# Optimization experiments

Measured on AMD Instinct MI355X. Metric: run time of the kernel, lower is better.

## Reference

```python
import jax, jax.numpy as jnp
import numpy as np

MAX_ITER = 10
TAU = 1.0


def setup_inputs() -> dict:
    key = jax.random.key(0)
    k1, k2, k3 = jax.random.split(key, 3)
    B, R, C = 64, 1024, 1024
    s = jax.random.normal(k1, (B, R, C), dtype=jnp.float32)
    # nrows <= ncols per batch => no transposed_batch branch in the original
    nrows = jax.random.randint(k2, (B,), 128, 512).astype(jnp.int32)
    ncols = jax.random.randint(k3, (B,), 512, C + 1).astype(jnp.int32)
    return {"s": s, "nrows": nrows, "ncols": ncols}


def _masked_lse(x, mask, axis):
    """logsumexp over `axis` restricted to mask==True; finite-safe everywhere.
    Equivalent to torch.logsumexp after writing -inf into masked-out entries,
    but keeps all values finite so grads are clean."""
    neg = jnp.asarray(-1e30, x.dtype)
    m = jax.lax.stop_gradient(jnp.max(jnp.where(mask, x, neg), axis=axis, keepdims=True))
    e = jnp.where(mask, jnp.exp(jnp.where(mask, x, m) - m), jnp.zeros((), x.dtype))
    sum_e = jnp.sum(e, axis=axis, keepdims=True)
    any_m = jnp.any(mask, axis=axis, keepdims=True)
    return m + jnp.log(jnp.where(any_m, sum_e, jnp.ones((), x.dtype)))


def _sinkhorn(s, nrows, ncols):
    B, R, C = s.shape
    row_mask = (jnp.arange(R)[None, :] < nrows[:, None])[:, :, None]  # [B,R,1]
    col_mask = (jnp.arange(C)[None, :] < ncols[:, None])[:, None, :]  # [B,1,C]
    valid = row_mask & col_mask                                        # [B,R,C]
    log_s = s / TAU
    # Alternating row/col normalization in log space. In the original, entries
    # outside [nrows,ncols] are set to -inf and ignored by logsumexp; here we
    # keep them finite and mask inside the logsumexp, which is the same math
    # on the valid region, and we zero the invalid region at the end (exp(-inf)=0).
    for i in range(MAX_ITER):
        if i % 2 == 0:  # row normalization
            lse = _masked_lse(log_s, valid, axis=2)          # [B,R,1]
            log_s = log_s - jnp.where(row_mask, lse, 0.0)
        else:           # col normalization
            lse = _masked_lse(log_s, valid, axis=1)          # [B,1,C]
            log_s = log_s - jnp.where(col_mask, lse, 0.0)
    return jnp.where(valid, jnp.exp(log_s), jnp.zeros((), s.dtype))


def reference(s, nrows, ncols):
    return _sinkhorn(s, nrows, ncols)
```

## Files before the change

kernel.cpp:

```cpp
#include <hip/hip_runtime.h>
#include <hip/hip_fp16.h>


#define B_DIM 64
#define RCH 32
#define NCH 16

__device__ __forceinline__ float fast_rcp(float x) {
#if __has_builtin(__builtin_amdgcn_rcpf)
    return __builtin_amdgcn_rcpf(x);
#else
    return 1.0f / x;
#endif
}

__device__ __forceinline__ float wave_sum(float x) {
    #pragma unroll
    for (int off = 1; off < 64; off <<= 1) x += __shfl_xor(x, off);
    return x;
}

__device__ __forceinline__ void phase2_col(
    const __half* __restrict__ E, const float* __restrict__ a_lds,
    float* __restrict__ cls,
    int b, int r0, int nr, int nc, int t, float* __restrict__ cs_cur)
{
    const int c0 = (t & 127) << 3;
    const int rsub = t >> 7;
    float acc0 = 0.f, acc1 = 0.f, acc2 = 0.f, acc3 = 0.f;
    float acc4 = 0.f, acc5 = 0.f, acc6 = 0.f, acc7 = 0.f;
    if (c0 < nc) {
        const int rs = r0 + (rsub << 3);
        const __half* __restrict__ Eb = E + ((size_t)b << 19) + c0;
        #pragma unroll
        for (int k = 0; k < 8; ++k) {
            const int r = rs + k;
            const float4 p = *reinterpret_cast<const float4*>(Eb + ((size_t)r << 10));
            const __half2* h = reinterpret_cast<const __half2*>(&p);
            const float av = a_lds[r - r0];
            const float2 f0 = __half22float2(h[0]);
            const float2 f1 = __half22float2(h[1]);
            const float2 f2 = __half22float2(h[2]);
            const float2 f3 = __half22float2(h[3]);
            acc0 = fmaf(f0.x, av, acc0); acc1 = fmaf(f0.y, av, acc1);
            acc2 = fmaf(f1.x, av, acc2); acc3 = fmaf(f1.y, av, acc3);
            acc4 = fmaf(f2.x, av, acc4); acc5 = fmaf(f2.y, av, acc5);
            acc6 = fmaf(f3.x, av, acc6); acc7 = fmaf(f3.y, av, acc7);
        }
    }
    float* dst = cls + (rsub << 10) + c0;
    *reinterpret_cast<float4*>(dst)     = make_float4(acc0, acc1, acc2, acc3);
    *reinterpret_cast<float4*>(dst + 4) = make_float4(acc4, acc5, acc6, acc7);
    __syncthreads();
    #pragma unroll
    for (int k = 0; k < 2; ++k) {
        const int c = t + (k << 9);
        const float v = cls[c] + cls[1024 + c] + cls[2048 + c] + cls[3072 + c];
        if (v != 0.f) atomicAdd(cs_cur + (b << 10) + c, v);
    }
}

__global__ __launch_bounds__(512) void pair_first(
    const float* __restrict__ s, const int* __restrict__ nrows,
    const int* __restrict__ ncols, __half* __restrict__ E,
    float* __restrict__ a, float* __restrict__ cs_cur,
    float* __restrict__ cs_next)
{
    const int b = blockIdx.y;
    const int rc = blockIdx.x;
    const int t = threadIdx.x;
    if (t < 64) cs_next[(b << 10) + (rc << 6) + t] = 0.f;

    const int nr = nrows[b];
    const int r0 = rc << 5;
    if (r0 >= nr) return;
    const int nc = ncols[b];

    __shared__ float a_lds[RCH];
    __shared__ float cls[4 * 1024];

    const int wave = t >> 6;
    const int lane = t & 63;
    const int cbase = lane << 4;
    const bool cOK = cbase < nc;

    #pragma unroll 1
    for (int k = 0; k < 4; ++k) {
        const int r = r0 + (wave << 2) + k;
        float sum = 0.f;
        if (r < nr && cOK) {
            const float* __restrict__ srow =
                s + ((size_t)b << 20) + ((size_t)r << 10) + cbase;
            __half* __restrict__ erow =
                E + ((size_t)b << 19) + ((size_t)r << 10) + cbase;
            float e[16];
            #pragma unroll
            for (int q = 0; q < 4; ++q) {
                const float4 x = *reinterpret_cast<const float4*>(srow + (q << 2));
                e[4 * q + 0] = __expf(x.x); e[4 * q + 1] = __expf(x.y);
                e[4 * q + 2] = __expf(x.z); e[4 * q + 3] = __expf(x.w);
            }
            #pragma unroll
            for (int j = 0; j < 16; ++j)
                if (cbase + j >= nc) e[j] = 0.f;
            __half2 h[8];
            #pragma unroll
            for (int q = 0; q < 8; ++q)
                h[q] = __floats2half2_rn(e[2 * q], e[2 * q + 1]);
            *reinterpret_cast<float4*>(erow)     = *reinterpret_cast<const float4*>(&h[0]);
            *reinterpret_cast<float4*>(erow + 8) = *reinterpret_cast<const float4*>(&h[4]);
            #pragma unroll
            for (int j = 0; j < 16; ++j) sum += e[j];
        }
        sum = wave_sum(sum);
        if (lane == 0) a_lds[(wave << 2) + k] = (r < nr) ? 1.0f / sum : 0.f;
    }
    __syncthreads();
    if (t < RCH) a[(b << 9) + r0 + t] = a_lds[t];

    phase2_col(E, a_lds, cls, b, r0, nr, nc, t, cs_cur);
}

__global__ __launch_bounds__(512) void pair_mid(
    const __half* __restrict__ E, const int* __restrict__ nrows,
    const int* __restrict__ ncols, const float* __restrict__ cs_prev,
    float* __restrict__ a, float* __restrict__ cs_cur,
    float* __restrict__ cs_next)
{
    const int b = blockIdx.y;
    const int rc = blockIdx.x;
    const int t = threadIdx.x;
    if (t < 64) cs_next[(b << 10) + (rc << 6) + t] = 0.f;

    const int nr = nrows[b];
    const int r0 = rc << 5;
    if (r0 >= nr) return;
    const int nc = ncols[b];

    __shared__ float a_lds[RCH];
    __shared__ float cls[4 * 1024];

    const int wave = t >> 6;
    const int lane = t & 63;
    const int cbase = lane << 4;
    const bool cOK = cbase < nc;

    float w[16];
    if (cOK) {
        const float* __restrict__ csp = cs_prev + (b << 10) + cbase;
        #pragma unroll
        for (int q = 0; q < 4; ++q) {
            const float4 c4 = *reinterpret_cast<const float4*>(csp + (q << 2));
            w[4 * q + 0] = (cbase + 4 * q + 0 < nc) ? fast_rcp(c4.x) : 0.f;
            w[4 * q + 1] = (cbase + 4 * q + 1 < nc) ? fast_rcp(c4.y) : 0.f;
            w[4 * q + 2] = (cbase + 4 * q + 2 < nc) ? fast_rcp(c4.z) : 0.f;
            w[4 * q + 3] = (cbase + 4 * q + 3 < nc) ? fast_rcp(c4.w) : 0.f;
        }
    }

    #pragma unroll 1
    for (int k = 0; k < 4; ++k) {
        const int r = r0 + (wave << 2) + k;
        float s0 = 0.f, s1 = 0.f;
        if (r < nr && cOK) {
            const __half* __restrict__ erow =
                E + ((size_t)b << 19) + ((size_t)r << 10) + cbase;
            float4 p0 = *reinterpret_cast<const float4*>(erow);
            float4 p1 = *reinterpret_cast<const float4*>(erow + 8);
            const __half2* h0 = reinterpret_cast<const __half2*>(&p0);
            const __half2* h1 = reinterpret_cast<const __half2*>(&p1);
            #pragma unroll
            for (int q = 0; q < 4; ++q) {
                const float2 f = __half22float2(h0[q]);
                s0 = fmaf(f.x, w[2 * q], s0);
                s1 = fmaf(f.y, w[2 * q + 1], s1);
            }
            #pragma unroll
            for (int q = 0; q < 4; ++q) {
                const float2 f = __half22float2(h1[q]);
                s0 = fmaf(f.x, w[8 + 2 * q], s0);
                s1 = fmaf(f.y, w[8 + 2 * q + 1], s1);
            }
        }
        const float sum = wave_sum(s0 + s1);
        if (lane == 0) a_lds[(wave << 2) + k] = (r < nr) ? 1.0f / sum : 0.f;
    }
    __syncthreads();
    if (t < RCH) a[(b << 9) + r0 + t] = a_lds[t];

    phase2_col(E, a_lds, cls, b, r0, nr, nc, t, cs_cur);
}

__global__ __launch_bounds__(256) void out_step_f(
    const __half* __restrict__ E, const int* __restrict__ nrows,
    const int* __restrict__ ncols, const float* __restrict__ a,
    const float* __restrict__ cs, float* __restrict__ out)
{
    const int g = (blockIdx.x << 8) + threadIdx.x;
    const int b = g >> 18;
    const int rem = g & 262143;
    const int r = rem >> 8;
    const int c0 = (rem & 255) << 2;
    const int nr = nrows[b];
    const int nc = ncols[b];
    float4 o = make_float4(0.f, 0.f, 0.f, 0.f);
    if (r < nr && c0 < nc) {
        const float ar = a[(b << 9) + r];
        float2 pk = *reinterpret_cast<const float2*>(
            E + ((size_t)b << 19) + ((size_t)r << 10) + c0);
        const float2 f01 = __half22float2(reinterpret_cast<const __half2*>(&pk)[0]);
        const float2 f23 = __half22float2(reinterpret_cast<const __half2*>(&pk)[1]);
        const float4 c4 = *reinterpret_cast<const float4*>(cs + (b << 10) + c0);
        o.x = f01.x * ar * fast_rcp(c4.x);
        o.y = (c0 + 1 < nc) ? f01.y * ar * fast_rcp(c4.y) : 0.f;
        o.z = (c0 + 2 < nc) ? f23.x * ar * fast_rcp(c4.z) : 0.f;
        o.w = (c0 + 3 < nc) ? f23.y * ar * fast_rcp(c4.w) : 0.f;
    }
    reinterpret_cast<float4*>(out)[g] = o;
}


__global__ __launch_bounds__(256) void row_step_lg(
    const float* __restrict__ s, const int* __restrict__ nrows,
    const int* __restrict__ ncols, const float* __restrict__ vlog,
    const int use_v, float* __restrict__ u)
{
    const int b = blockIdx.y, r = blockIdx.x;
    const int nr = nrows[b];
    if (r >= nr) return;
    const int nc = ncols[b];
    const int t = threadIdx.x, c0 = t << 2;
    float sum = 0.f;
    if (c0 < nc) {
        const float4 x = reinterpret_cast<const float4*>(
            s + ((size_t)b << 20) + ((size_t)r << 10))[t];
        float4 vv = make_float4(0.f, 0.f, 0.f, 0.f);
        if (use_v) vv = reinterpret_cast<const float4*>(vlog + ((size_t)b << 10))[t];
        sum  = (c0 + 0 < nc) ? __expf(x.x - vv.x) : 0.f;
        sum += (c0 + 1 < nc) ? __expf(x.y - vv.y) : 0.f;
        sum += (c0 + 2 < nc) ? __expf(x.z - vv.z) : 0.f;
        sum += (c0 + 3 < nc) ? __expf(x.w - vv.w) : 0.f;
    }
    #pragma unroll
    for (int off = 1; off < 64; off <<= 1) sum += __shfl_xor(sum, off);
    __shared__ float ss[4];
    if ((t & 63) == 0) ss[t >> 6] = sum;
    __syncthreads();
    if (t == 0) u[((size_t)b << 9) + r] = __logf(ss[0] + ss[1] + ss[2] + ss[3]);
}

__global__ __launch_bounds__(256) void col_step_lg(
    const float* __restrict__ s, const int* __restrict__ nrows,
    const int* __restrict__ ncols, const float* __restrict__ u,
    float* __restrict__ partial)
{
    const int b = blockIdx.z, rc = blockIdx.y;
    const int nr = nrows[b];
    const int r0 = rc << 6;
    if (r0 >= nr) return;
    const int nc = ncols[b];
    const int c = (blockIdx.x << 8) + threadIdx.x;
    float sum = 0.f;
    if (c < nc) {
        const int rend = min(r0 + 64, nr);
        const float* __restrict__ sb = s + ((size_t)b << 20) + c;
        const float* __restrict__ ub = u + ((size_t)b << 9);
        float s0 = 0.f, s1 = 0.f, s2 = 0.f, s3 = 0.f;
        int r = r0;
        for (; r + 4 <= rend; r += 4) {
            s0 += __expf(sb[(size_t)(r + 0) << 10] - ub[r + 0]);
            s1 += __expf(sb[(size_t)(r + 1) << 10] - ub[r + 1]);
            s2 += __expf(sb[(size_t)(r + 2) << 10] - ub[r + 2]);
            s3 += __expf(sb[(size_t)(r + 3) << 10] - ub[r + 3]);
        }
        for (; r < rend; ++r) s0 += __expf(sb[(size_t)r << 10] - ub[r]);
        sum = (s0 + s1) + (s2 + s3);
    }
    partial[(((size_t)b << 3) + rc) << 10 | c] = sum;
}

__global__ __launch_bounds__(256) void col_fin_lg(
    const int* __restrict__ nrows, const float* __restrict__ partial,
    float* __restrict__ vlog)
{
    const int idx = (blockIdx.x << 8) + threadIdx.x;
    const int b = idx >> 10;
    const int nch = (nrows[b] + 63) >> 6;
    const float* __restrict__ p = partial + ((size_t)(b << 3) << 10) + (idx & 1023);
    float sum = 0.f;
    for (int k = 0; k < nch; ++k) sum += p[(size_t)k << 10];
    vlog[idx] = (sum > 0.f) ? __logf(sum) : 0.f;
}

__global__ __launch_bounds__(256) void out_step_lg(
    const float* __restrict__ s, const int* __restrict__ nrows,
    const int* __restrict__ ncols, const float* __restrict__ u,
    const float* __restrict__ vlog, float* __restrict__ out)
{
    const size_t total4 = (size_t)B_DIM * 1024 * 1024 / 4;
    float4* out4 = reinterpret_cast<float4*>(out);
    const float4* s4 = reinterpret_cast<const float4*>(s);
    for (size_t i = (size_t)blockIdx.x * blockDim.x + threadIdx.x; i < total4;
         i += (size_t)gridDim.x * blockDim.x) {
        const int b = (int)(i >> 18);
        const int rem = (int)(i & 262143);
        const int r = rem >> 8;
        const int c0 = (rem & 255) << 2;
        const int nr = nrows[b], nc = ncols[b];
        float4 o;
        if (r >= nr || c0 >= nc) {
            o = make_float4(0.f, 0.f, 0.f, 0.f);
        } else {
            float4 x = s4[i];
            const float ur = u[((size_t)b << 9) + r];
            const float* vb = vlog + ((size_t)b << 10);
            o.x = (c0 + 0 < nc) ? __expf(x.x - ur - vb[c0 + 0]) : 0.f;
            o.y = (c0 + 1 < nc) ? __expf(x.y - ur - vb[c0 + 1]) : 0.f;
            o.z = (c0 + 2 < nc) ? __expf(x.z - ur - vb[c0 + 2]) : 0.f;
            o.w = (c0 + 3 < nc) ? __expf(x.w - ur - vb[c0 + 3]) : 0.f;
        }
        out4[i] = o;
    }
}


extern "C" void kernel_launch(void* const* d_in, const int* in_sizes, int n_in,
                              void* d_out, int out_size, void* d_ws, size_t ws_size,
                              hipStream_t stream) {
    const float* s = (const float*)d_in[0];
    const int* nrows = (const int*)d_in[1];
    const int* ncols = (const int*)d_in[2];
    float* out = (float*)d_out;

    const size_t E_BYTES = (size_t)B_DIM * 512 * 1024 * 2;
    const size_t CS_ELEMS = (size_t)B_DIM * 1024;
    const size_t NEED = E_BYTES + (size_t)B_DIM * 512 * 4 + 3 * CS_ELEMS * 4;

    if (ws_size >= NEED) {
        __half* E = (__half*)d_ws;
        float* a = (float*)((char*)d_ws + E_BYTES);
        float* cs0 = a + B_DIM * 512;
        float* cs1 = cs0 + CS_ELEMS;
        float* cs2 = cs1 + CS_ELEMS;

        hipMemsetAsync(cs0, 0, CS_ELEMS * sizeof(float), stream);

        const dim3 grid(NCH, B_DIM);
        pair_first<<<grid, 512, 0, stream>>>(s, nrows, ncols, E, a, cs0, cs1);
        pair_mid<<<grid, 512, 0, stream>>>(E, nrows, ncols, cs0, a, cs1, cs2);
        pair_mid<<<grid, 512, 0, stream>>>(E, nrows, ncols, cs1, a, cs2, cs0);
        pair_mid<<<grid, 512, 0, stream>>>(E, nrows, ncols, cs2, a, cs0, cs1);
        pair_mid<<<grid, 512, 0, stream>>>(E, nrows, ncols, cs0, a, cs1, cs2);
        out_step_f<<<65536, 256, 0, stream>>>(E, nrows, ncols, a, cs1, out);
    } else {
        float* u = (float*)d_ws;
        float* vlog = u + (size_t)B_DIM * 512;
        float* partial = vlog + (size_t)B_DIM * 1024;
        const dim3 rowGrid(512, B_DIM);
        const dim3 colGrid(4, 8, B_DIM);
        for (int it = 0; it < 5; ++it) {
            row_step_lg<<<rowGrid, 256, 0, stream>>>(s, nrows, ncols, vlog, it, u);
            col_step_lg<<<colGrid, 256, 0, stream>>>(s, nrows, ncols, u, partial);
            col_fin_lg<<<256, 256, 0, stream>>>(nrows, partial, vlog);
        }
        out_step_lg<<<4096, 256, 0, stream>>>(s, nrows, ncols, u, vlog, out);
    }
}
```

Baseline: 161.4 us.

## Stage E tile in LDS for column pass and swizzle blocks across XCDs

The row pass now writes its 32x1024 fp16 tile of E into shared memory, and the column-sum phase reads from LDS instead of reloading E from global memory. This removes the second global or L2 read of each tile per iteration. Block indices are also remapped so each XCD handles a contiguous group of batches, for L2 locality in both the pair kernels and the output kernel. The LDS footprint grows to 64KB per block, which may limit occupancy. Each thread now issues two atomics instead of the previous LDS pre-reduction.

```diff
diff --git a/kernel.cpp b/kernel.cpp
--- a/kernel.cpp
+++ b/kernel.cpp
@@ -4,7 +4,6 @@
 
 #define B_DIM 64
 #define RCH 32
-#define NCH 16
 
 __device__ __forceinline__ float fast_rcp(float x) {
 #if __has_builtin(__builtin_amdgcn_rcpf)
@@ -21,43 +20,30 @@
 }
 
 __device__ __forceinline__ void phase2_col(
-    const __half* __restrict__ E, const float* __restrict__ a_lds,
-    float* __restrict__ cls,
-    int b, int r0, int nr, int nc, int t, float* __restrict__ cs_cur)
-{
-    const int c0 = (t & 127) << 3;
-    const int rsub = t >> 7;
-    float acc0 = 0.f, acc1 = 0.f, acc2 = 0.f, acc3 = 0.f;
-    float acc4 = 0.f, acc5 = 0.f, acc6 = 0.f, acc7 = 0.f;
-    if (c0 < nc) {
-        const int rs = r0 + (rsub << 3);
-        const __half* __restrict__ Eb = E + ((size_t)b << 19) + c0;
-        #pragma unroll
-        for (int k = 0; k < 8; ++k) {
-            const int r = rs + k;
-            const float4 p = *reinterpret_cast<const float4*>(Eb + ((size_t)r << 10));
-            const __half2* h = reinterpret_cast<const __half2*>(&p);
-            const float av = a_lds[r - r0];
-            const float2 f0 = __half22float2(h[0]);
-            const float2 f1 = __half22float2(h[1]);
-            const float2 f2 = __half22float2(h[2]);
-            const float2 f3 = __half22float2(h[3]);
-            acc0 = fmaf(f0.x, av, acc0); acc1 = fmaf(f0.y, av, acc1);
-            acc2 = fmaf(f1.x, av, acc2); acc3 = fmaf(f1.y, av, acc3);
-            acc4 = fmaf(f2.x, av, acc4); acc5 = fmaf(f2.y, av, acc5);
-            acc6 = fmaf(f3.x, av, acc6); acc7 = fmaf(f3.y, av, acc7);
-        }
-    }
-    float* dst = cls + (rsub << 10) + c0;
-    *reinterpret_cast<float4*>(dst)     = make_float4(acc0, acc1, acc2, acc3);
-    *reinterpret_cast<float4*>(dst + 4) = make_float4(acc4, acc5, acc6, acc7);
-    __syncthreads();
+    const __half* __restrict__ e_lds,
+    const float* __restrict__ a_lds, int b, int nc, int t,
+    float* __restrict__ cs_cur)
+{
+    const int c0 = t << 1;
+    if (c0 >= nc) return;
+    float s0 = 0.f, s1 = 0.f;
     #pragma unroll
-    for (int k = 0; k < 2; ++k) {
-        const int c = t + (k << 9);
-        const float v = cls[c] + cls[1024 + c] + cls[2048 + c] + cls[3072 + c];
-        if (v != 0.f) atomicAdd(cs_cur + (b << 10) + c, v);
-    }
+    for (int rr = 0; rr < RCH; ++rr) {
+        const float2 f = __half22float2(
+            *reinterpret_cast<const __half2*>(e_lds + (rr << 10) + c0));
+        const float av = a_lds[rr];
+        s0 = fmaf(f.x, av, s0);
+        s1 = fmaf(f.y, av, s1);
+    }
+    if (s0 != 0.f) atomicAdd(cs_cur + (b << 10) + c0, s0);
+    if (s1 != 0.f) atomicAdd(cs_cur + (b << 10) + c0 + 1, s1);
+}
+
+__device__ __forceinline__ void decode_pair_bid(int bid, int& b, int& rc) {
+    const int xcd = bid & 7;
+    const int j = bid >> 3;
+    rc = j & 15;
+    b = (xcd << 3) | (j >> 4);
 }
 
 __global__ __launch_bounds__(512) void pair_first(
@@ -66,8 +52,8 @@
     float* __restrict__ a, float* __restrict__ cs_cur,
     float* __restrict__ cs_next)
 {
-    const int b = blockIdx.y;
-    const int rc = blockIdx.x;
+    int b, rc;
+    decode_pair_bid(blockIdx.x, b, rc);
     const int t = threadIdx.x;
     if (t < 64) cs_next[(b << 10) + (rc << 6) + t] = 0.f;
 
@@ -76,8 +62,8 @@
     if (r0 >= nr) return;
     const int nc = ncols[b];
 
+    __shared__ __half e_lds[RCH * 1024];
     __shared__ float a_lds[RCH];
-    __shared__ float cls[4 * 1024];
 
     const int wave = t >> 6;
     const int lane = t & 63;
@@ -86,13 +72,13 @@
 
     #pragma unroll 1
     for (int k = 0; k < 4; ++k) {
-        const int r = r0 + (wave << 2) + k;
+        const int rr = (wave << 2) + k;
+        const int r = r0 + rr;
         float sum = 0.f;
+        __half2 h[8];
         if (r < nr && cOK) {
             const float* __restrict__ srow =
                 s + ((size_t)b << 20) + ((size_t)r << 10) + cbase;
-            __half* __restrict__ erow =
-                E + ((size_t)b << 19) + ((size_t)r << 10) + cbase;
             float e[16];
             #pragma unroll
             for (int q = 0; q < 4; ++q) {
@@ -103,22 +89,29 @@
             #pragma unroll
             for (int j = 0; j < 16; ++j)
                 if (cbase + j >= nc) e[j] = 0.f;
-            __half2 h[8];
             #pragma unroll
             for (int q = 0; q < 8; ++q)
                 h[q] = __floats2half2_rn(e[2 * q], e[2 * q + 1]);
+            __half* __restrict__ erow =
+                E + ((size_t)b << 19) + ((size_t)r << 10) + cbase;
             *reinterpret_cast<float4*>(erow)     = *reinterpret_cast<const float4*>(&h[0]);
             *reinterpret_cast<float4*>(erow + 8) = *reinterpret_cast<const float4*>(&h[4]);
             #pragma unroll
             for (int j = 0; j < 16; ++j) sum += e[j];
-        }
+        } else {
+            #pragma unroll
+            for (int q = 0; q < 8; ++q) h[q] = __floats2half2_rn(0.f, 0.f);
+        }
+        __half* dst = e_lds + (rr << 10) + cbase;
+        *reinterpret_cast<float4*>(dst)     = *reinterpret_cast<const float4*>(&h[0]);
+        *reinterpret_cast<float4*>(dst + 8) = *reinterpret_cast<const float4*>(&h[4]);
         sum = wave_sum(sum);
-        if (lane == 0) a_lds[(wave << 2) + k] = (r < nr) ? 1.0f / sum : 0.f;
+        if (lane == 0) a_lds[rr] = (r < nr) ? 1.0f / sum : 0.f;
     }
     __syncthreads();
     if (t < RCH) a[(b << 9) + r0 + t] = a_lds[t];
 
-    phase2_col(E, a_lds, cls, b, r0, nr, nc, t, cs_cur);
+    phase2_col(e_lds, a_lds, b, nc, t, cs_cur);
 }
 
 __global__ __launch_bounds__(512) void pair_mid(
@@ -127,8 +120,8 @@
     float* __restrict__ a, float* __restrict__ cs_cur,
     float* __restrict__ cs_next)
 {
-    const int b = blockIdx.y;
-    const int rc = blockIdx.x;
+    int b, rc;
+    decode_pair_bid(blockIdx.x, b, rc);
     const int t = threadIdx.x;
     if (t < 64) cs_next[(b << 10) + (rc << 6) + t] = 0.f;
 
@@ -137,8 +130,8 @@
     if (r0 >= nr) return;
     const int nc = ncols[b];
 
+    __shared__ __half e_lds[RCH * 1024];
     __shared__ float a_lds[RCH];
-    __shared__ float cls[4 * 1024];
 
     const int wave = t >> 6;
     const int lane = t & 63;
@@ -160,13 +153,15 @@
 
     #pragma unroll 1
     for (int k = 0; k < 4; ++k) {
-        const int r = r0 + (wave << 2) + k;
+        const int rr = (wave << 2) + k;
+        const int r = r0 + rr;
         float s0 = 0.f, s1 = 0.f;
+        float4 p0, p1;
         if (r < nr && cOK) {
             const __half* __restrict__ erow =
                 E + ((size_t)b << 19) + ((size_t)r << 10) + cbase;
-            float4 p0 = *reinterpret_cast<const float4*>(erow);
-            float4 p1 = *reinterpret_cast<const float4*>(erow + 8);
+            p0 = *reinterpret_cast<const float4*>(erow);
+            p1 = *reinterpret_cast<const float4*>(erow + 8);
             const __half2* h0 = reinterpret_cast<const __half2*>(&p0);
             const __half2* h1 = reinterpret_cast<const __half2*>(&p1);
             #pragma unroll
@@ -181,14 +176,20 @@
                 s0 = fmaf(f.x, w[8 + 2 * q], s0);
                 s1 = fmaf(f.y, w[8 + 2 * q + 1], s1);
             }
-        }
+        } else {
+            p0 = make_float4(0.f, 0.f, 0.f, 0.f);
+            p1 = p0;
+        }
+        __half* dst = e_lds + (rr << 10) + cbase;
+        *reinterpret_cast<float4*>(dst)     = p0;
+        *reinterpret_cast<float4*>(dst + 8) = p1;
         const float sum = wave_sum(s0 + s1);
-        if (lane == 0) a_lds[(wave << 2) + k] = (r < nr) ? 1.0f / sum : 0.f;
+        if (lane == 0) a_lds[rr] = (r < nr) ? 1.0f / sum : 0.f;
     }
     __syncthreads();
     if (t < RCH) a[(b << 9) + r0 + t] = a_lds[t];
 
-    phase2_col(E, a_lds, cls, b, r0, nr, nc, t, cs_cur);
+    phase2_col(e_lds, a_lds, b, nc, t, cs_cur);
 }
 
 __global__ __launch_bounds__(256) void out_step_f(
@@ -196,11 +197,13 @@
     const int* __restrict__ ncols, const float* __restrict__ a,
     const float* __restrict__ cs, float* __restrict__ out)
 {
-    const int g = (blockIdx.x << 8) + threadIdx.x;
-    const int b = g >> 18;
-    const int rem = g & 262143;
-    const int r = rem >> 8;
-    const int c0 = (rem & 255) << 2;
+    const int bid = blockIdx.x;
+    const int xcd = bid & 7;
+    const int j = bid >> 3;
+    const int r = j & 1023;
+    const int b = (xcd << 3) | (j >> 10);
+    const int c0 = threadIdx.x << 2;
+
     const int nr = nrows[b];
     const int nc = ncols[b];
     float4 o = make_float4(0.f, 0.f, 0.f, 0.f);
@@ -216,7 +219,7 @@
         o.z = (c0 + 2 < nc) ? f23.x * ar * fast_rcp(c4.z) : 0.f;
         o.w = (c0 + 3 < nc) ? f23.y * ar * fast_rcp(c4.w) : 0.f;
     }
-    reinterpret_cast<float4*>(out)[g] = o;
+    *reinterpret_cast<float4*>(out + ((size_t)b << 20) + ((size_t)r << 10) + c0) = o;
 }
 
 
@@ -345,12 +348,12 @@
 
         hipMemsetAsync(cs0, 0, CS_ELEMS * sizeof(float), stream);
 
-        const dim3 grid(NCH, B_DIM);
-        pair_first<<<grid, 512, 0, stream>>>(s, nrows, ncols, E, a, cs0, cs1);
-        pair_mid<<<grid, 512, 0, stream>>>(E, nrows, ncols, cs0, a, cs1, cs2);
-        pair_mid<<<grid, 512, 0, stream>>>(E, nrows, ncols, cs1, a, cs2, cs0);
-        pair_mid<<<grid, 512, 0, stream>>>(E, nrows, ncols, cs2, a, cs0, cs1);
-        pair_mid<<<grid, 512, 0, stream>>>(E, nrows, ncols, cs0, a, cs1, cs2);
+        const int nblk = 16 * B_DIM;
+        pair_first<<<nblk, 512, 0, stream>>>(s, nrows, ncols, E, a, cs0, cs1);
+        pair_mid<<<nblk, 512, 0, stream>>>(E, nrows, ncols, cs0, a, cs1, cs2);
+        pair_mid<<<nblk, 512, 0, stream>>>(E, nrows, ncols, cs1, a, cs2, cs0);
+        pair_mid<<<nblk, 512, 0, stream>>>(E, nrows, ncols, cs2, a, cs0, cs1);
+        pair_mid<<<nblk, 512, 0, stream>>>(E, nrows, ncols, cs0, a, cs1, cs2);
         out_step_f<<<65536, 256, 0, stream>>>(E, nrows, ncols, a, cs1, out);
     } else {
         float* u = (float*)d_ws;
```

New measurement: 162.9 us. Within noise of the previous version (+1.0%).
